# Kernel optimization log

Hardware: AMD Instinct MI355X
Metric: run time of the kernel (lower is better)

The kernel has to match this reference:

```python
import jax, jax.numpy as jnp
from jax import lax
import numpy as np

NODE = 100000
D = 256      # input_dim
H = 256      # hidden_dim
P = 4096     # num paths between the pair
L = 8        # path length (hops)
OUT = 1


def setup_inputs() -> dict:
    key = jax.random.key(0)
    ks = jax.random.split(key, 10)
    s = 1.0 / np.sqrt(H)
    return {
        "embedding": jax.random.normal(ks[0], (NODE, D), jnp.float32) * 0.1,
        "w_ih": jax.random.normal(ks[1], (4 * H, D), jnp.float32) * s,
        "w_hh": jax.random.normal(ks[2], (4 * H, H), jnp.float32) * s,
        "b_ih": jax.random.normal(ks[3], (4 * H,), jnp.float32) * s,
        "b_hh": jax.random.normal(ks[4], (4 * H,), jnp.float32) * s,
        "w_lin": jax.random.normal(ks[5], (OUT, H + 2 * D), jnp.float32) * 0.05,
        "b_lin": jax.random.normal(ks[6], (OUT,), jnp.float32) * 0.05,
        "paths": jax.random.randint(ks[7], (P, L), 0, NODE, jnp.int64),
        "user_id": jax.random.randint(ks[8], (1,), 0, NODE, jnp.int64),
        "item_id": jax.random.randint(ks[9], (1,), 0, NODE, jnp.int64),
    }


def _lstm_final_hidden(x, w_ih, w_hh, b_ih, b_hh):
    # x: [P, L, D] -> final hidden state h_n: [P, H] (PyTorch gate order i,f,g,o)
    p, _, _ = x.shape
    h = x.shape  # noqa (shape comment)
    hidden = w_hh.shape[1]
    b = b_ih + b_hh

    def step(carry, x_t):
        h, c = carry
        gates = x_t @ w_ih.T + h @ w_hh.T + b  # [P, 4H]
        i, f, g, o = jnp.split(gates, 4, axis=-1)
        c = jax.nn.sigmoid(f) * c + jax.nn.sigmoid(i) * jnp.tanh(g)
        h = jax.nn.sigmoid(o) * jnp.tanh(c)
        return (h, c), None

    h0 = jnp.zeros((p, hidden), x.dtype)
    c0 = jnp.zeros((p, hidden), x.dtype)
    (h_n, _), _ = lax.scan(step, (h0, c0), jnp.swapaxes(x, 0, 1))  # scan over L
    return h_n


def reference(embedding, w_ih, w_hh, b_ih, b_hh, w_lin, b_lin, paths, user_id, item_id):
    # Batched version of the per-path loop: embed all paths, one LSTM scan.
    x = embedding[paths]                                   # [P, L, D]
    sum_hidden = _lstm_final_hidden(x, w_ih, w_hh, b_ih, b_hh)  # [P, H] (== stacked h_n)

    # MaxPool2d((1, H)) over hidden dim -> attention logits over paths
    att = jnp.max(sum_hidden, axis=-1, keepdims=True)      # [P, 1]
    att = jax.nn.softmax(att, axis=0)                      # softmax over paths
    path_emb = jnp.sum(sum_hidden * att, axis=0, keepdims=True)  # [1, H]

    user_emb = embedding[user_id]                          # [1, D]
    item_emb = embedding[item_id]                          # [1, D]
    emb = jnp.concatenate([user_emb, item_emb, path_emb], axis=-1)  # [1, 2D+H]
    out = jax.nn.sigmoid(emb @ w_lin.T + b_lin)            # [1, OUT]
    return out
```

## Files before the change

### kernel.cpp

```cpp
#include <hip/hip_runtime.h>
#include <stdint.h>

#define NPATHS 4096
#define LPATH  8
#define DIM    256
#define HID    256

typedef short  short4v __attribute__((ext_vector_type(4)));
typedef short  short8v __attribute__((ext_vector_type(8)));
typedef float  float4v __attribute__((ext_vector_type(4)));

__device__ __forceinline__ unsigned short f2bf(float f) {
    union { float f; uint32_t u; } v; v.f = f;
    uint32_t u = v.u;
    u += 0x7FFFu + ((u >> 16) & 1u);
    return (unsigned short)(u >> 16);
}
__device__ __forceinline__ float bf2f(unsigned short s) {
    return __uint_as_float(((uint32_t)s) << 16);
}
__device__ __forceinline__ float fast_sigmoid(float x) {
    return 1.0f / (1.0f + __expf(-x));
}
__device__ __forceinline__ float fast_tanh(float x) {
    x = fminf(15.0f, fmaxf(-15.0f, x));
    float e = __expf(2.0f * x);
    return (e - 1.0f) / (e + 1.0f);
}
__device__ __forceinline__ unsigned int encf(float f) {
    unsigned int u = __float_as_uint(f);
    return (u & 0x80000000u) ? ~u : (u | 0x80000000u);
}
__device__ __forceinline__ float decf(unsigned int u) {
    return (u & 0x80000000u) ? __uint_as_float(u & 0x7FFFFFFFu) : __uint_as_float(~u);
}

__device__ __forceinline__ void dma16(void* lds, const void* g) {
    typedef const unsigned int __attribute__((address_space(1)))* gp_t;
    typedef unsigned int __attribute__((address_space(3)))* lp_t;
    gp_t gp = reinterpret_cast<gp_t>(reinterpret_cast<uintptr_t>(g));
    lp_t lp = reinterpret_cast<lp_t>(static_cast<unsigned int>(reinterpret_cast<uintptr_t>(lds)));
    __builtin_amdgcn_global_load_lds(gp, lp, 16, 0, 0);
}

__global__ void prep_gather(const float* __restrict__ w_ih, const float* __restrict__ w_hh,
                            const float* __restrict__ b_ih, const float* __restrict__ b_hh,
                            const float* __restrict__ embedding, const int* __restrict__ paths,
                            unsigned short* __restrict__ WfB, float* __restrict__ bias,
                            unsigned int* __restrict__ logits_enc, float* __restrict__ path_emb,
                            unsigned short* __restrict__ Xb) {
    int bid = blockIdx.x;
    if (bid < 512) {
        int gid  = bid * 256 + threadIdx.x;
        int base = gid * 4;
        int j0   = base & 31;
        int unit = (base >> 5) & 255;
        int gkc  = base >> 13;
        int g    = gkc >> 4, kc = gkc & 15;
        int row  = g * 256 + unit;
        int k    = kc * 32 + j0;
        const float* src = (k < DIM) ? (w_ih + (size_t)row * DIM + k)
                                     : (w_hh + (size_t)row * HID + (k - DIM));
        float4 v = *(const float4*)src;
        short4v pk = {(short)f2bf(v.x), (short)f2bf(v.y), (short)f2bf(v.z), (short)f2bf(v.w)};
        *(short4v*)(WfB + base) = pk;
        if (gid < 1024) bias[gid] = b_ih[gid] + b_hh[gid];
        if (gid < NPATHS) logits_enc[gid] = 0u;
        if (gid < 256) path_emb[gid] = 0.0f;
    } else {
        int gid  = (bid - 512) * 256 + threadIdx.x;
        int rowt = gid >> 6;
        int seg  = gid & 63;
        int p    = rowt & (NPATHS - 1);
        int t    = rowt >> 12;
        int node = paths[p * LPATH + t];
        float4 v = *(const float4*)(embedding + (size_t)node * DIM + seg * 4);
        short4v pk = {(short)f2bf(v.x), (short)f2bf(v.y), (short)f2bf(v.z), (short)f2bf(v.w)};
        *(short4v*)(Xb + (size_t)rowt * DIM + seg * 4) = pk;
    }
}

template<bool FIRST, bool LAST>
__global__ __launch_bounds__(256, 1)
void step_kernel(const unsigned short* __restrict__ Xb,
                 const unsigned short* __restrict__ WfB,
                 const float* __restrict__ bias,
                 const unsigned short* __restrict__ h_in,
                 unsigned short* __restrict__ h_out,
                 float* __restrict__ c_g,
                 unsigned int* __restrict__ logits_enc,
                 int t) {
    __shared__ __align__(16) short sA[64 * 512];

    const int tid   = threadIdx.x;
    const int wave  = tid >> 6;
    const int lane  = tid & 63;
    const int l15   = lane & 15;
    const int quad  = lane >> 4;
    const int blk   = blockIdx.x;
    const int ptile = blk & 63;
    const int utile = blk >> 6;
    const int p0    = ptile * 64;
    const int u0    = utile * 64;

    {
        const char* xpl = (const char*)Xb + ((size_t)t * NPATHS + p0) * 512;
        const char* hpl = (const char*)h_in + (size_t)p0 * 512;
        const char* xl  = xpl + l15 * 512 + quad * 16;
        const char* hl  = hpl + l15 * 512 + quad * 16;
#pragma unroll
        for (int m = 0; m < 16; ++m) {
            int rf = m >> 2, kq = m & 3;
            if (FIRST && kq >= 2) continue;
            int fp = rf * 16 + kq * 4 + wave;
            const char* base = (kq < 2) ? xl : hl;
            int kk = ((kq & 1) * 4 + wave) * 64;
            dma16(sA + fp * 512, base + rf * 8192 + kk);
        }
    }

    short8v Bf[4][16];
    float bb[4];
    const int unit = u0 + wave * 16 + l15;
#pragma unroll
    for (int g = 0; g < 4; ++g) {
        bb[g] = bias[g * 256 + unit];
#pragma unroll
        for (int kc = 0; kc < 16; ++kc)
            Bf[g][kc] = *(const short8v*)(WfB + (((g * 16 + kc) * 256 + unit) * 32 + quad * 8));
    }

    __syncthreads();

    float4v acc[4][4];
    const float4v z4 = {0.0f, 0.0f, 0.0f, 0.0f};
#pragma unroll
    for (int rf = 0; rf < 4; ++rf)
#pragma unroll
        for (int g = 0; g < 4; ++g) acc[rf][g] = z4;

    auto kstep = [&](int kc) {
#pragma unroll
        for (int rf = 0; rf < 4; ++rf) {
            short8v a = *(const short8v*)(sA + ((rf * 16 + kc) << 9) + lane * 8);
#pragma unroll
            for (int g = 0; g < 4; ++g)
                acc[rf][g] = __builtin_amdgcn_mfma_f32_16x16x32_bf16(
                    a, Bf[g][kc], acc[rf][g], 0, 0, 0);
        }
    };
    if (FIRST) {
#pragma unroll
        for (int kc = 0; kc < 8; ++kc) kstep(kc);
    } else {
#pragma unroll
        for (int kc = 0; kc < 16; ++kc) kstep(kc);
    }

    float hmax[16];
#pragma unroll
    for (int rf = 0; rf < 4; ++rf) {
#pragma unroll
        for (int r = 0; r < 4; ++r) {
            int row = rf * 16 + quad * 4 + r;
            int idx = rf * 4 + r;
            float iv = acc[rf][0][r] + bb[0];
            float fv = acc[rf][1][r] + bb[1];
            float gv = acc[rf][2][r] + bb[2];
            float ov = acc[rf][3][r] + bb[3];
            size_t coff = (size_t)(p0 + row) * HID + unit;
            float cp = FIRST ? 0.0f : c_g[coff];
            float cn = fast_sigmoid(fv) * cp + fast_sigmoid(iv) * fast_tanh(gv);
            if (!LAST) c_g[coff] = cn;
            float h = fast_sigmoid(ov) * fast_tanh(cn);
            hmax[idx] = h;
            h_out[(size_t)(p0 + row) * HID + unit] = f2bf(h);
        }
    }

    if (LAST) {
#pragma unroll
        for (int idx = 0; idx < 16; ++idx) {
            float m = hmax[idx];
            m = fmaxf(m, __shfl_xor(m, 1, 64));
            m = fmaxf(m, __shfl_xor(m, 2, 64));
            m = fmaxf(m, __shfl_xor(m, 4, 64));
            m = fmaxf(m, __shfl_xor(m, 8, 64));
            if (l15 == 0) {
                int rf = idx >> 2, r = idx & 3;
                atomicMax(&logits_enc[p0 + rf * 16 + quad * 4 + r], encf(m));
            }
        }
    }
}

__global__ void softmax_prep_kernel(const unsigned int* __restrict__ enc,
                                    float* __restrict__ scal) {
    __shared__ float red[256];
    int tid = threadIdx.x;
    float vals[16];
    float m = -1e30f;
#pragma unroll
    for (int i = 0; i < 16; ++i) {
        vals[i] = decf(enc[i * 256 + tid]);
        m = fmaxf(m, vals[i]);
    }
    red[tid] = m; __syncthreads();
    for (int s = 128; s > 0; s >>= 1) {
        if (tid < s) red[tid] = fmaxf(red[tid], red[tid + s]);
        __syncthreads();
    }
    m = red[0]; __syncthreads();
    float sum = 0.0f;
#pragma unroll
    for (int i = 0; i < 16; ++i) sum += __expf(vals[i] - m);
    red[tid] = sum; __syncthreads();
    for (int s = 128; s > 0; s >>= 1) {
        if (tid < s) red[tid] += red[tid + s];
        __syncthreads();
    }
    if (tid == 0) { scal[0] = m; scal[1] = 1.0f / red[0]; }
}

__global__ void attn_sum_kernel(const unsigned short* __restrict__ h_final,
                                const unsigned int* __restrict__ enc,
                                const float* __restrict__ scal,
                                float* __restrict__ path_emb) {
    int tid = threadIdx.x;
    int p0  = blockIdx.x * 16;
    float bmax = scal[0], invZ = scal[1];
    float acc = 0.0f;
    for (int p = p0; p < p0 + 16; ++p) {
        float w = __expf(decf(enc[p]) - bmax) * invZ;
        acc += w * bf2f(h_final[(size_t)p * HID + tid]);
    }
    atomicAdd(&path_emb[tid], acc);
}

__global__ void final_kernel(const float* __restrict__ embedding,
                             const int* __restrict__ user_id,
                             const int* __restrict__ item_id,
                             const float* __restrict__ w_lin,
                             const float* __restrict__ b_lin,
                             const float* __restrict__ path_emb,
                             float* __restrict__ out) {
    __shared__ float red[256];
    int tid = threadIdx.x;
    int u  = user_id[0];
    int it = item_id[0];
    float s = w_lin[tid]       * embedding[(size_t)u  * DIM + tid]
            + w_lin[256 + tid] * embedding[(size_t)it * DIM + tid]
            + w_lin[512 + tid] * path_emb[tid];
    red[tid] = s; __syncthreads();
    for (int st = 128; st > 0; st >>= 1) {
        if (tid < st) red[tid] += red[tid + st];
        __syncthreads();
    }
    if (tid == 0) out[0] = 1.0f / (1.0f + __expf(-(red[0] + b_lin[0])));
}

extern "C" void kernel_launch(void* const* d_in, const int* in_sizes, int n_in,
                              void* d_out, int out_size, void* d_ws, size_t ws_size,
                              hipStream_t stream) {
    const float* embedding = (const float*)d_in[0];
    const float* w_ih      = (const float*)d_in[1];
    const float* w_hh      = (const float*)d_in[2];
    const float* b_ih      = (const float*)d_in[3];
    const float* b_hh      = (const float*)d_in[4];
    const float* w_lin     = (const float*)d_in[5];
    const float* b_lin     = (const float*)d_in[6];
    const int*   paths     = (const int*)d_in[7];
    const int*   user_id   = (const int*)d_in[8];
    const int*   item_id   = (const int*)d_in[9];
    float* outp = (float*)d_out;

    char* ws = (char*)d_ws;
    size_t off = 0;
    auto alloc = [&](size_t n) { void* p = ws + off; off = (off + n + 255) & ~(size_t)255; return p; };
    unsigned short* WfB       = (unsigned short*)alloc((size_t)1024 * 512 * 2);
    float*          bias      = (float*)alloc(1024 * 4);
    unsigned int*   logits_enc= (unsigned int*)alloc(NPATHS * 4);
    float*          scal      = (float*)alloc(256);
    float*          path_emb  = (float*)alloc(HID * 4);
    unsigned short* Xb        = (unsigned short*)alloc((size_t)LPATH * NPATHS * DIM * 2);
    unsigned short* h_buf     = (unsigned short*)alloc((size_t)2 * NPATHS * HID * 2);
    float*          c_g       = (float*)alloc((size_t)NPATHS * HID * 4);

    prep_gather<<<8704, 256, 0, stream>>>(w_ih, w_hh, b_ih, b_hh, embedding, paths,
                                          WfB, bias, logits_enc, path_emb, Xb);

    for (int t = 0; t < LPATH; ++t) {
        const unsigned short* hin = h_buf + (size_t)(t & 1) * NPATHS * HID;
        unsigned short*      hout = h_buf + (size_t)((t + 1) & 1) * NPATHS * HID;
        if (t == 0)
            step_kernel<true, false><<<256, 256, 0, stream>>>(Xb, WfB, bias, hin, hout,
                                                              c_g, logits_enc, t);
        else if (t == LPATH - 1)
            step_kernel<false, true><<<256, 256, 0, stream>>>(Xb, WfB, bias, hin, hout,
                                                              c_g, logits_enc, t);
        else
            step_kernel<false, false><<<256, 256, 0, stream>>>(Xb, WfB, bias, hin, hout,
                                                               c_g, logits_enc, t);
    }

    softmax_prep_kernel<<<1, 256, 0, stream>>>(logits_enc, scal);
    attn_sum_kernel<<<NPATHS / 16, 256, 0, stream>>>(h_buf, logits_enc, scal, path_emb);
    final_kernel<<<1, 256, 0, stream>>>(embedding, user_id, item_id, w_lin, b_lin,
                                        path_emb, outp);
}
```

Baseline: 276.4 us.

## Fuse LSTM steps and epilogue into one persistent kernel with grid barriers

Replaces the eight per-timestep kernel launches and the three tail kernels with a single persistent kernel of 256 blocks that synchronise through a software grid barrier. Weight fragments are loaded into registers once, and the cell state stays in registers instead of round-tripping through global memory. The h tile is staged through LDS so it is written to global memory with coalesced vector stores. The softmax, attention sum and final linear layer run in the same kernel. The cost is spin-wait barriers, which rely on all 256 blocks being co-resident and could deadlock otherwise. The epilogue also serialises on block 0.

```diff
diff --git a/kernel.cpp b/kernel.cpp
--- a/kernel.cpp
+++ b/kernel.cpp
@@ -5,6 +5,7 @@
 #define LPATH  8
 #define DIM    256
 #define HID    256
+#define NBLK   256
 
 typedef short  short4v __attribute__((ext_vector_type(4)));
 typedef short  short8v __attribute__((ext_vector_type(8)));
@@ -15,9 +16,6 @@
     uint32_t u = v.u;
     u += 0x7FFFu + ((u >> 16) & 1u);
     return (unsigned short)(u >> 16);
-}
-__device__ __forceinline__ float bf2f(unsigned short s) {
-    return __uint_as_float(((uint32_t)s) << 16);
 }
 __device__ __forceinline__ float fast_sigmoid(float x) {
     return 1.0f / (1.0f + __expf(-x));
@@ -43,12 +41,30 @@
     __builtin_amdgcn_global_load_lds(gp, lp, 16, 0, 0);
 }
 
+__device__ __forceinline__ void grid_barrier(unsigned int* cnt, unsigned int* gen, int tid) {
+    __syncthreads();
+    if (tid == 0) {
+        __threadfence();
+        unsigned int g = __hip_atomic_load(gen, __ATOMIC_RELAXED, __HIP_MEMORY_SCOPE_AGENT);
+        unsigned int a = __hip_atomic_fetch_add(cnt, 1u, __ATOMIC_ACQ_REL, __HIP_MEMORY_SCOPE_AGENT);
+        if (a == NBLK - 1) {
+            __hip_atomic_store(cnt, 0u, __ATOMIC_RELAXED, __HIP_MEMORY_SCOPE_AGENT);
+            __hip_atomic_fetch_add(gen, 1u, __ATOMIC_ACQ_REL, __HIP_MEMORY_SCOPE_AGENT);
+        } else {
+            while (__hip_atomic_load(gen, __ATOMIC_RELAXED, __HIP_MEMORY_SCOPE_AGENT) == g)
+                __builtin_amdgcn_s_sleep(2);
+        }
+        __threadfence();
+    }
+    __syncthreads();
+}
+
 __global__ void prep_gather(const float* __restrict__ w_ih, const float* __restrict__ w_hh,
                             const float* __restrict__ b_ih, const float* __restrict__ b_hh,
                             const float* __restrict__ embedding, const int* __restrict__ paths,
                             unsigned short* __restrict__ WfB, float* __restrict__ bias,
                             unsigned int* __restrict__ logits_enc, float* __restrict__ path_emb,
-                            unsigned short* __restrict__ Xb) {
+                            unsigned short* __restrict__ Xb, unsigned int* __restrict__ bar) {
     int bid = blockIdx.x;
     if (bid < 512) {
         int gid  = bid * 256 + threadIdx.x;
@@ -67,6 +83,7 @@
         if (gid < 1024) bias[gid] = b_ih[gid] + b_hh[gid];
         if (gid < NPATHS) logits_enc[gid] = 0u;
         if (gid < 256) path_emb[gid] = 0.0f;
+        if (gid < 2) bar[gid] = 0u;
     } else {
         int gid  = (bid - 512) * 256 + threadIdx.x;
         int rowt = gid >> 6;
@@ -80,17 +97,26 @@
     }
 }
 
-template<bool FIRST, bool LAST>
 __global__ __launch_bounds__(256, 1)
-void step_kernel(const unsigned short* __restrict__ Xb,
-                 const unsigned short* __restrict__ WfB,
-                 const float* __restrict__ bias,
-                 const unsigned short* __restrict__ h_in,
-                 unsigned short* __restrict__ h_out,
-                 float* __restrict__ c_g,
-                 unsigned int* __restrict__ logits_enc,
-                 int t) {
+void lstm_persist(const unsigned short* __restrict__ Xb,
+                  const unsigned short* __restrict__ WfB,
+                  const float* __restrict__ bias,
+                  unsigned short* __restrict__ h_buf,
+                  unsigned int* __restrict__ logits_enc,
+                  float* __restrict__ pw,
+                  float* __restrict__ path_emb,
+                  const float* __restrict__ embedding,
+                  const int* __restrict__ user_id,
+                  const int* __restrict__ item_id,
+                  const float* __restrict__ w_lin,
+                  const float* __restrict__ b_lin,
+                  float* __restrict__ out,
+                  unsigned int* __restrict__ bar) {
     __shared__ __align__(16) short sA[64 * 512];
+    short* hT  = sA;
+    float* red = (float*)sA;
+    unsigned int* bcnt = bar;
+    unsigned int* bgen = bar + 1;
 
     const int tid   = threadIdx.x;
     const int wave  = tid >> 6;
@@ -103,22 +129,6 @@
     const int p0    = ptile * 64;
     const int u0    = utile * 64;
 
-    {
-        const char* xpl = (const char*)Xb + ((size_t)t * NPATHS + p0) * 512;
-        const char* hpl = (const char*)h_in + (size_t)p0 * 512;
-        const char* xl  = xpl + l15 * 512 + quad * 16;
-        const char* hl  = hpl + l15 * 512 + quad * 16;
-#pragma unroll
-        for (int m = 0; m < 16; ++m) {
-            int rf = m >> 2, kq = m & 3;
-            if (FIRST && kq >= 2) continue;
-            int fp = rf * 16 + kq * 4 + wave;
-            const char* base = (kq < 2) ? xl : hl;
-            int kk = ((kq & 1) * 4 + wave) * 64;
-            dma16(sA + fp * 512, base + rf * 8192 + kk);
-        }
-    }
-
     short8v Bf[4][16];
     float bb[4];
     const int unit = u0 + wave * 16 + l15;
@@ -130,133 +140,154 @@
             Bf[g][kc] = *(const short8v*)(WfB + (((g * 16 + kc) * 256 + unit) * 32 + quad * 8));
     }
 
-    __syncthreads();
-
-    float4v acc[4][4];
-    const float4v z4 = {0.0f, 0.0f, 0.0f, 0.0f};
-#pragma unroll
-    for (int rf = 0; rf < 4; ++rf)
-#pragma unroll
-        for (int g = 0; g < 4; ++g) acc[rf][g] = z4;
-
-    auto kstep = [&](int kc) {
+    float c_reg[16], h_reg[16];
+#pragma unroll
+    for (int i = 0; i < 16; ++i) c_reg[i] = 0.0f;
+
+    for (int t = 0; t < LPATH; ++t) {
+        {
+            const char* xpl = (const char*)Xb + ((size_t)t * NPATHS + p0) * 512;
+            const char* hpl = (const char*)h_buf + ((size_t)(t & 1) * NPATHS + p0) * 512;
+            const char* xl  = xpl + l15 * 512 + quad * 16;
+            const char* hl  = hpl + l15 * 512 + quad * 16;
+#pragma unroll
+            for (int m = 0; m < 16; ++m) {
+                int rf = m >> 2, kq = m & 3;
+                if (t == 0 && kq >= 2) continue;
+                int fp = rf * 16 + kq * 4 + wave;
+                const char* base = (kq < 2) ? xl : hl;
+                int kk = ((kq & 1) * 4 + wave) * 64;
+                dma16(sA + fp * 512, base + rf * 8192 + kk);
+            }
+        }
+        __syncthreads();
+
+        float4v acc[4][4];
+        const float4v z4 = {0.0f, 0.0f, 0.0f, 0.0f};
+#pragma unroll
+        for (int rf = 0; rf < 4; ++rf)
+#pragma unroll
+            for (int g = 0; g < 4; ++g) acc[rf][g] = z4;
+
+        auto kstep = [&](int kc) {
+#pragma unroll
+            for (int rf = 0; rf < 4; ++rf) {
+                short8v a = *(const short8v*)(sA + ((rf * 16 + kc) << 9) + lane * 8);
+#pragma unroll
+                for (int g = 0; g < 4; ++g)
+                    acc[rf][g] = __builtin_amdgcn_mfma_f32_16x16x32_bf16(
+                        a, Bf[g][kc], acc[rf][g], 0, 0, 0);
+            }
+        };
+        const int nkc = (t == 0) ? 8 : 16;
+        for (int kc = 0; kc < nkc; ++kc) kstep(kc);
+
 #pragma unroll
         for (int rf = 0; rf < 4; ++rf) {
-            short8v a = *(const short8v*)(sA + ((rf * 16 + kc) << 9) + lane * 8);
-#pragma unroll
-            for (int g = 0; g < 4; ++g)
-                acc[rf][g] = __builtin_amdgcn_mfma_f32_16x16x32_bf16(
-                    a, Bf[g][kc], acc[rf][g], 0, 0, 0);
-        }
-    };
-    if (FIRST) {
-#pragma unroll
-        for (int kc = 0; kc < 8; ++kc) kstep(kc);
-    } else {
-#pragma unroll
-        for (int kc = 0; kc < 16; ++kc) kstep(kc);
-    }
-
-    float hmax[16];
-#pragma unroll
-    for (int rf = 0; rf < 4; ++rf) {
-#pragma unroll
-        for (int r = 0; r < 4; ++r) {
-            int row = rf * 16 + quad * 4 + r;
-            int idx = rf * 4 + r;
-            float iv = acc[rf][0][r] + bb[0];
-            float fv = acc[rf][1][r] + bb[1];
-            float gv = acc[rf][2][r] + bb[2];
-            float ov = acc[rf][3][r] + bb[3];
-            size_t coff = (size_t)(p0 + row) * HID + unit;
-            float cp = FIRST ? 0.0f : c_g[coff];
-            float cn = fast_sigmoid(fv) * cp + fast_sigmoid(iv) * fast_tanh(gv);
-            if (!LAST) c_g[coff] = cn;
-            float h = fast_sigmoid(ov) * fast_tanh(cn);
-            hmax[idx] = h;
-            h_out[(size_t)(p0 + row) * HID + unit] = f2bf(h);
-        }
-    }
-
-    if (LAST) {
-#pragma unroll
-        for (int idx = 0; idx < 16; ++idx) {
-            float m = hmax[idx];
-            m = fmaxf(m, __shfl_xor(m, 1, 64));
-            m = fmaxf(m, __shfl_xor(m, 2, 64));
-            m = fmaxf(m, __shfl_xor(m, 4, 64));
-            m = fmaxf(m, __shfl_xor(m, 8, 64));
-            if (l15 == 0) {
-                int rf = idx >> 2, r = idx & 3;
-                atomicMax(&logits_enc[p0 + rf * 16 + quad * 4 + r], encf(m));
-            }
-        }
-    }
-}
-
-__global__ void softmax_prep_kernel(const unsigned int* __restrict__ enc,
-                                    float* __restrict__ scal) {
-    __shared__ float red[256];
-    int tid = threadIdx.x;
-    float vals[16];
-    float m = -1e30f;
-#pragma unroll
-    for (int i = 0; i < 16; ++i) {
-        vals[i] = decf(enc[i * 256 + tid]);
-        m = fmaxf(m, vals[i]);
-    }
-    red[tid] = m; __syncthreads();
-    for (int s = 128; s > 0; s >>= 1) {
-        if (tid < s) red[tid] = fmaxf(red[tid], red[tid + s]);
-        __syncthreads();
-    }
-    m = red[0]; __syncthreads();
-    float sum = 0.0f;
-#pragma unroll
-    for (int i = 0; i < 16; ++i) sum += __expf(vals[i] - m);
-    red[tid] = sum; __syncthreads();
-    for (int s = 128; s > 0; s >>= 1) {
-        if (tid < s) red[tid] += red[tid + s];
-        __syncthreads();
-    }
-    if (tid == 0) { scal[0] = m; scal[1] = 1.0f / red[0]; }
-}
-
-__global__ void attn_sum_kernel(const unsigned short* __restrict__ h_final,
-                                const unsigned int* __restrict__ enc,
-                                const float* __restrict__ scal,
-                                float* __restrict__ path_emb) {
-    int tid = threadIdx.x;
-    int p0  = blockIdx.x * 16;
-    float bmax = scal[0], invZ = scal[1];
-    float acc = 0.0f;
-    for (int p = p0; p < p0 + 16; ++p) {
-        float w = __expf(decf(enc[p]) - bmax) * invZ;
-        acc += w * bf2f(h_final[(size_t)p * HID + tid]);
-    }
-    atomicAdd(&path_emb[tid], acc);
-}
-
-__global__ void final_kernel(const float* __restrict__ embedding,
-                             const int* __restrict__ user_id,
-                             const int* __restrict__ item_id,
-                             const float* __restrict__ w_lin,
-                             const float* __restrict__ b_lin,
-                             const float* __restrict__ path_emb,
-                             float* __restrict__ out) {
-    __shared__ float red[256];
-    int tid = threadIdx.x;
-    int u  = user_id[0];
-    int it = item_id[0];
-    float s = w_lin[tid]       * embedding[(size_t)u  * DIM + tid]
-            + w_lin[256 + tid] * embedding[(size_t)it * DIM + tid]
-            + w_lin[512 + tid] * path_emb[tid];
-    red[tid] = s; __syncthreads();
-    for (int st = 128; st > 0; st >>= 1) {
-        if (tid < st) red[tid] += red[tid + st];
-        __syncthreads();
-    }
-    if (tid == 0) out[0] = 1.0f / (1.0f + __expf(-(red[0] + b_lin[0])));
+#pragma unroll
+            for (int r = 0; r < 4; ++r) {
+                int idx = rf * 4 + r;
+                float iv = acc[rf][0][r] + bb[0];
+                float fv = acc[rf][1][r] + bb[1];
+                float gv = acc[rf][2][r] + bb[2];
+                float ov = acc[rf][3][r] + bb[3];
+                float cn = fast_sigmoid(fv) * c_reg[idx]
+                         + fast_sigmoid(iv) * fast_tanh(gv);
+                c_reg[idx] = cn;
+                h_reg[idx] = fast_sigmoid(ov) * fast_tanh(cn);
+            }
+        }
+
+        if (t < LPATH - 1) {
+            __syncthreads();
+#pragma unroll
+            for (int rf = 0; rf < 4; ++rf)
+#pragma unroll
+                for (int r = 0; r < 4; ++r)
+                    hT[(rf * 16 + quad * 4 + r) * 72 + wave * 16 + l15] =
+                        (short)f2bf(h_reg[rf * 4 + r]);
+            __syncthreads();
+            unsigned short* hdst = h_buf + (size_t)((t + 1) & 1) * NPATHS * HID
+                                 + (size_t)p0 * HID + u0;
+#pragma unroll
+            for (int i = 0; i < 2; ++i) {
+                int cid = i * 256 + tid;
+                int row = cid >> 3, seg = cid & 7;
+                short8v v = *(const short8v*)(hT + row * 72 + seg * 8);
+                *(short8v*)(hdst + (size_t)row * HID + seg * 8) = v;
+            }
+        } else {
+#pragma unroll
+            for (int idx = 0; idx < 16; ++idx) {
+                float m = h_reg[idx];
+                m = fmaxf(m, __shfl_xor(m, 1, 64));
+                m = fmaxf(m, __shfl_xor(m, 2, 64));
+                m = fmaxf(m, __shfl_xor(m, 4, 64));
+                m = fmaxf(m, __shfl_xor(m, 8, 64));
+                if (l15 == 0) {
+                    int rf = idx >> 2, r = idx & 3;
+                    atomicMax(&logits_enc[p0 + rf * 16 + quad * 4 + r], encf(m));
+                }
+            }
+        }
+        grid_barrier(bcnt, bgen, tid);
+    }
+
+    if (blk == 0) {
+        float vals[16];
+        float m = -1e30f;
+#pragma unroll
+        for (int i = 0; i < 16; ++i) {
+            vals[i] = decf(logits_enc[i * 256 + tid]);
+            m = fmaxf(m, vals[i]);
+        }
+        red[tid] = m; __syncthreads();
+        for (int s = 128; s > 0; s >>= 1) {
+            if (tid < s) red[tid] = fmaxf(red[tid], red[tid + s]);
+            __syncthreads();
+        }
+        m = red[0]; __syncthreads();
+        float e[16];
+        float sum = 0.0f;
+#pragma unroll
+        for (int i = 0; i < 16; ++i) { e[i] = __expf(vals[i] - m); sum += e[i]; }
+        red[tid] = sum; __syncthreads();
+        for (int s = 128; s > 0; s >>= 1) {
+            if (tid < s) red[tid] += red[tid + s];
+            __syncthreads();
+        }
+        float invZ = 1.0f / red[0];
+#pragma unroll
+        for (int i = 0; i < 16; ++i) pw[i * 256 + tid] = e[i] * invZ;
+    }
+    grid_barrier(bcnt, bgen, tid);
+
+    {
+        float s = 0.0f;
+#pragma unroll
+        for (int rf = 0; rf < 4; ++rf)
+#pragma unroll
+            for (int r = 0; r < 4; ++r)
+                s += pw[p0 + rf * 16 + quad * 4 + r] * h_reg[rf * 4 + r];
+        s += __shfl_xor(s, 16, 64);
+        s += __shfl_xor(s, 32, 64);
+        if (quad == 0) atomicAdd(&path_emb[unit], s);
+    }
+    grid_barrier(bcnt, bgen, tid);
+
+    if (blk == 0) {
+        int u  = user_id[0];
+        int it = item_id[0];
+        float s = w_lin[tid]       * embedding[(size_t)u  * DIM + tid]
+                + w_lin[256 + tid] * embedding[(size_t)it * DIM + tid]
+                + w_lin[512 + tid] * path_emb[tid];
+        red[tid] = s; __syncthreads();
+        for (int st = 128; st > 0; st >>= 1) {
+            if (tid < st) red[tid] += red[tid + st];
+            __syncthreads();
+        }
+        if (tid == 0) out[0] = 1.0f / (1.0f + __expf(-(red[0] + b_lin[0])));
+    }
 }
 
 extern "C" void kernel_launch(void* const* d_in, const int* in_sizes, int n_in,
@@ -280,31 +311,16 @@
     unsigned short* WfB       = (unsigned short*)alloc((size_t)1024 * 512 * 2);
     float*          bias      = (float*)alloc(1024 * 4);
     unsigned int*   logits_enc= (unsigned int*)alloc(NPATHS * 4);
-    float*          scal      = (float*)alloc(256);
+    float*          pw        = (float*)alloc(NPATHS * 4);
     float*          path_emb  = (float*)alloc(HID * 4);
+    unsigned int*   bar       = (unsigned int*)alloc(256);
     unsigned short* Xb        = (unsigned short*)alloc((size_t)LPATH * NPATHS * DIM * 2);
     unsigned short* h_buf     = (unsigned short*)alloc((size_t)2 * NPATHS * HID * 2);
-    float*          c_g       = (float*)alloc((size_t)NPATHS * HID * 4);
 
     prep_gather<<<8704, 256, 0, stream>>>(w_ih, w_hh, b_ih, b_hh, embedding, paths,
-                                          WfB, bias, logits_enc, path_emb, Xb);
-
-    for (int t = 0; t < LPATH; ++t) {
-        const unsigned short* hin = h_buf + (size_t)(t & 1) * NPATHS * HID;
-        unsigned short*      hout = h_buf + (size_t)((t + 1) & 1) * NPATHS * HID;
-        if (t == 0)
-            step_kernel<true, false><<<256, 256, 0, stream>>>(Xb, WfB, bias, hin, hout,
-                                                              c_g, logits_enc, t);
-        else if (t == LPATH - 1)
-            step_kernel<false, true><<<256, 256, 0, stream>>>(Xb, WfB, bias, hin, hout,
-                                                              c_g, logits_enc, t);
-        else
-            step_kernel<false, false><<<256, 256, 0, stream>>>(Xb, WfB, bias, hin, hout,
-                                                               c_g, logits_enc, t);
-    }
-
-    softmax_prep_kernel<<<1, 256, 0, stream>>>(logits_enc, scal);
-    attn_sum_kernel<<<NPATHS / 16, 256, 0, stream>>>(h_buf, logits_enc, scal, path_emb);
-    final_kernel<<<1, 256, 0, stream>>>(embedding, user_id, item_id, w_lin, b_lin,
-                                        path_emb, outp);
-}
+                                          WfB, bias, logits_enc, path_emb, Xb, bar);
+
+    lstm_persist<<<NBLK, 256, 0, stream>>>(Xb, WfB, bias, h_buf, logits_enc, pw, path_emb,
+                                           embedding, user_id, item_id, w_lin, b_lin,
+                                           outp, bar);
+}
```

Measured after the change: 582.9 us. 111% more time.
